# Optimization experiments

Hardware: AMD Instinct MI355X
Metric: run time of the kernel (lower is better)

## Reference

```python
import jax, jax.numpy as jnp
import numpy as np

B, OUT, IN = 4096, 1024, 1024
BN_EPS = 1e-5


def setup_inputs() -> dict:
    key = jax.random.key(0)
    kx, k1, k2, k3 = jax.random.split(key, 4)
    # kaiming_uniform_ with a=sqrt(5): bound = sqrt(6 / ((1+a^2) * fan_in)) = 1/sqrt(fan_in)
    bound = 1.0 / np.sqrt(IN)
    x = jax.random.normal(kx, (B, IN), dtype=jnp.float32)
    c1 = jax.random.uniform(k1, (OUT, IN), jnp.float32, -bound, bound)
    c2 = jax.random.uniform(k2, (OUT, IN), jnp.float32, -bound, bound)
    c3 = jax.random.uniform(k3, (OUT, IN), jnp.float32, -bound, bound)
    bias = jnp.zeros((OUT, IN), jnp.float32)
    gamma = jnp.ones((OUT,), jnp.float32)   # BatchNorm1d weight
    beta = jnp.zeros((OUT,), jnp.float32)   # BatchNorm1d bias
    return {"x": x, "c1": c1, "c2": c2, "c3": c3, "bias": bias,
            "gamma": gamma, "beta": beta}


def reference(x, c1, c2, c3, bias, gamma, beta):
    # Fused polynomial 'matmul': out[b,o] = sum_i x*c1 + x^2*c2 + x^3*c3 + bias
    x2 = x * x
    x3 = x2 * x
    y = (jnp.einsum('bi,oi->bo', x, c1)
         + jnp.einsum('bi,oi->bo', x2, c2)
         + jnp.einsum('bi,oi->bo', x3, c3)
         + jnp.sum(bias, axis=1))  # bias reduced over in_features
    # BatchNorm1d (training mode: batch statistics, biased variance)
    mean = jnp.mean(y, axis=0)
    var = jnp.var(y, axis=0)
    return (y - mean) * jax.lax.rsqrt(var + BN_EPS) * gamma + beta
```

## Files before the change

kernel.cpp:

```cpp
#include <hip/hip_runtime.h>
#include <stdint.h>

#define B_ROWS 4096
#define OUTF   1024
#define INF    1024
#define KTOT   3072
#define BN_EPS 1e-5f
#define BM 128
#define BN 64
#define BK 128

typedef short  short8  __attribute__((ext_vector_type(8)));
typedef float  floatx4 __attribute__((ext_vector_type(4)));

struct alignas(8) s4 { short x, y, z, w; };

__device__ __forceinline__ short f2bf(float f) {
  union { float f; uint32_t u; } cv; cv.f = f;
  uint32_t u = cv.u;
  uint32_t r = (u + 0x7fffu + ((u >> 16) & 1u)) >> 16;
  return (short)r;
}

__device__ __forceinline__ void load_lds16(const void* g, void* l) {
  __builtin_amdgcn_global_load_lds(
      (const __attribute__((address_space(1))) uint32_t*)(uintptr_t)g,
      (__attribute__((address_space(3))) uint32_t*)(uint32_t)(uintptr_t)l,
      16, 0, 0);
}

__global__ void prep_all(const float4* __restrict__ x4,
                         const float4* __restrict__ c1, const float4* __restrict__ c2,
                         const float4* __restrict__ c3, const float* __restrict__ bias,
                         short* __restrict__ Xb, short* __restrict__ Wb,
                         float* __restrict__ biassum) {
  int b = blockIdx.x;
  if (b < 4096) {
    int idx = b * 256 + threadIdx.x;
    float4 v = x4[idx];
    int row = idx >> 8;
    int c   = (idx & 255) << 2;
    size_t base = (size_t)row * KTOT + c;
    s4 p1 = { f2bf(v.x), f2bf(v.y), f2bf(v.z), f2bf(v.w) };
    float ax = v.x * v.x, ay = v.y * v.y, az = v.z * v.z, aw = v.w * v.w;
    s4 p2 = { f2bf(ax), f2bf(ay), f2bf(az), f2bf(aw) };
    s4 p3 = { f2bf(ax * v.x), f2bf(ay * v.y), f2bf(az * v.z), f2bf(aw * v.w) };
    *(s4*)&Xb[base]        = p1;
    *(s4*)&Xb[base + 1024] = p2;
    *(s4*)&Xb[base + 2048] = p3;
  } else if (b < 5120) {
    int idx = (b - 4096) * 256 + threadIdx.x;
    int row = idx >> 8;
    int c   = (idx & 255) << 2;
    size_t base = (size_t)row * KTOT + c;
    float4 a = c1[idx], bb = c2[idx], d = c3[idx];
    s4 p1 = { f2bf(a.x),  f2bf(a.y),  f2bf(a.z),  f2bf(a.w)  };
    s4 p2 = { f2bf(bb.x), f2bf(bb.y), f2bf(bb.z), f2bf(bb.w) };
    s4 p3 = { f2bf(d.x),  f2bf(d.y),  f2bf(d.z),  f2bf(d.w)  };
    *(s4*)&Wb[base]        = p1;
    *(s4*)&Wb[base + 1024] = p2;
    *(s4*)&Wb[base + 2048] = p3;
  } else {
    int o = (b - 5120) * 4 + (threadIdx.x >> 6);
    int l = threadIdx.x & 63;
    const float4* bp = (const float4*)(bias + (size_t)o * INF);
    float s = 0.f;
    for (int i = l; i < 256; i += 64) { float4 v = bp[i]; s += v.x + v.y + v.z + v.w; }
    #pragma unroll
    for (int off = 32; off; off >>= 1) s += __shfl_down(s, off, 64);
    if (l == 0) biassum[o] = s;
  }
}

__global__ __launch_bounds__(256, 2) void gemm_poly(
    const short* __restrict__ Xb, const short* __restrict__ Wb,
    const float* __restrict__ biassum, float* __restrict__ Y,
    float* __restrict__ psum, float* __restrict__ psq) {
  __shared__ __align__(16) short As[BM * BK];
  __shared__ __align__(16) short Bs[BN * BK];
  __shared__ float colred[2][2][BN];
  const int tid  = threadIdx.x;
  const int lane = tid & 63;
  const int wave = tid >> 6;
  const int wr = wave >> 1;
  const int wc = wave & 1;
  const int row0 = blockIdx.y * BM;
  const int col0 = blockIdx.x * BN;
  const short* Ag = Xb + (size_t)row0 * KTOT;
  const short* Bg = Wb + (size_t)col0 * KTOT;
  const int frag_m = lane & 15;
  const int sel = lane >> 4;
  floatx4 acc[4][2] = {};

  int aoff[8], boff[4];
  #pragma unroll
  for (int i = 0; i < 8; ++i) {
    int c = tid + i * 256;
    int r = c >> 4, p = c & 15;
    int l = p ^ (r & 15);
    aoff[i] = r * KTOT + l * 8;
  }
  #pragma unroll
  for (int i = 0; i < 4; ++i) {
    int c = tid + i * 256;
    int r = c >> 4, p = c & 15;
    int l = p ^ (r & 15);
    boff[i] = r * KTOT + l * 8;
  }

  for (int kt = 0; kt < KTOT; kt += BK) {
    #pragma unroll
    for (int i = 0; i < 8; ++i)
      load_lds16(Ag + aoff[i] + kt, &As[(tid + i * 256) * 8]);
    #pragma unroll
    for (int i = 0; i < 4; ++i)
      load_lds16(Bg + boff[i] + kt, &Bs[(tid + i * 256) * 8]);
    __syncthreads();
    #pragma unroll
    for (int s = 0; s < 4; ++s) {
      short8 af[4], bfr[2];
      #pragma unroll
      for (int i = 0; i < 4; ++i) {
        int r = wr * 64 + i * 16 + frag_m;
        int p = (s * 4 + sel) ^ (r & 15);
        af[i] = *(const short8*)&As[r * BK + p * 8];
      }
      #pragma unroll
      for (int j = 0; j < 2; ++j) {
        int r = wc * 32 + j * 16 + frag_m;
        int p = (s * 4 + sel) ^ (r & 15);
        bfr[j] = *(const short8*)&Bs[r * BK + p * 8];
      }
      #pragma unroll
      for (int i = 0; i < 4; ++i)
        #pragma unroll
        for (int j = 0; j < 2; ++j)
          acc[i][j] = __builtin_amdgcn_mfma_f32_16x16x32_bf16(af[i], bfr[j], acc[i][j], 0, 0, 0);
    }
    __syncthreads();
  }

  const int drow = (lane >> 4) << 2;
  const int dcol = lane & 15;
  float s[2] = {0.f, 0.f}, sq[2] = {0.f, 0.f};
  #pragma unroll
  for (int j = 0; j < 2; ++j) {
    int gc = col0 + wc * 32 + j * 16 + dcol;
    float bsv = biassum[gc];
    #pragma unroll
    for (int i = 0; i < 4; ++i) {
      int gr = row0 + wr * 64 + i * 16 + drow;
      #pragma unroll
      for (int r = 0; r < 4; ++r) {
        float v = acc[i][j][r] + bsv;
        Y[(size_t)(gr + r) * OUTF + gc] = v;
        s[j] += v; sq[j] += v * v;
      }
    }
  }
  #pragma unroll
  for (int j = 0; j < 2; ++j) {
    s[j]  += __shfl_xor(s[j], 16, 64);  s[j]  += __shfl_xor(s[j], 32, 64);
    sq[j] += __shfl_xor(sq[j], 16, 64); sq[j] += __shfl_xor(sq[j], 32, 64);
  }
  if (sel == 0) {
    #pragma unroll
    for (int j = 0; j < 2; ++j) {
      int cc = wc * 32 + j * 16 + dcol;
      colred[wr][0][cc] = s[j];
      colred[wr][1][cc] = sq[j];
    }
  }
  __syncthreads();
  if (tid < BN) {
    psum[(size_t)blockIdx.y * OUTF + col0 + tid] = colred[0][0][tid] + colred[1][0][tid];
    psq [(size_t)blockIdx.y * OUTF + col0 + tid] = colred[0][1][tid] + colred[1][1][tid];
  }
}

__global__ void bn_fused(const float* __restrict__ psum, const float* __restrict__ psq,
                         const float* __restrict__ gamma, const float* __restrict__ beta,
                         float* __restrict__ Y) {
  __shared__ float sc[32], sh[32];
  const int c0 = blockIdx.x * 32;
  const int t = threadIdx.x;
  if (t < 32) {
    float s = 0.f, s2 = 0.f;
    #pragma unroll 8
    for (int p = 0; p < 32; ++p) {
      s  += psum[p * OUTF + c0 + t];
      s2 += psq [p * OUTF + c0 + t];
    }
    float mean = s * (1.0f / B_ROWS);
    float var  = s2 * (1.0f / B_ROWS) - mean * mean;
    float scale = gamma[c0 + t] * rsqrtf(var + BN_EPS);
    sc[t] = scale;
    sh[t] = beta[c0 + t] - mean * scale;
  }
  __syncthreads();
  const int f4c = t & 7;
  const int rr  = t >> 3;
  const int row0 = blockIdx.y * 256;
  float4* Y4 = (float4*)Y;
  const int cb = f4c * 4;
  float s0 = sc[cb], s1 = sc[cb+1], s2 = sc[cb+2], s3 = sc[cb+3];
  float h0 = sh[cb], h1 = sh[cb+1], h2 = sh[cb+2], h3 = sh[cb+3];
  #pragma unroll
  for (int it = 0; it < 8; ++it) {
    int row = row0 + it * 32 + rr;
    size_t idx = (size_t)row * 256 + (c0 >> 2) + f4c;
    float4 v = Y4[idx];
    v.x = v.x * s0 + h0; v.y = v.y * s1 + h1;
    v.z = v.z * s2 + h2; v.w = v.w * s3 + h3;
    Y4[idx] = v;
  }
}

extern "C" void kernel_launch(void* const* d_in, const int* in_sizes, int n_in,
                              void* d_out, int out_size, void* d_ws, size_t ws_size,
                              hipStream_t stream) {
  const float* x     = (const float*)d_in[0];
  const float* c1    = (const float*)d_in[1];
  const float* c2    = (const float*)d_in[2];
  const float* c3    = (const float*)d_in[3];
  const float* bias  = (const float*)d_in[4];
  const float* gamma = (const float*)d_in[5];
  const float* beta  = (const float*)d_in[6];
  float* out = (float*)d_out;
  char* ws = (char*)d_ws;

  short* Xb      = (short*)(ws);
  short* Wb      = (short*)(ws + 25165824);
  float* biassum = (float*)(ws + 31457280);
  float* psum    = (float*)(ws + 31461376);
  float* psq     = (float*)(ws + 31592448);

  prep_all<<<5376, 256, 0, stream>>>((const float4*)x, (const float4*)c1,
                                     (const float4*)c2, (const float4*)c3,
                                     bias, Xb, Wb, biassum);

  dim3 ggrid(OUTF / BN, B_ROWS / BM);
  gemm_poly<<<ggrid, 256, 0, stream>>>(Xb, Wb, biassum, out, psum, psq);

  dim3 bgrid(OUTF / 32, B_ROWS / 256);
  bn_fused<<<bgrid, 256, 0, stream>>>(psum, psq, gamma, beta, out);
}
```

Measured before the change: 136.0 us.

## Double-buffer LDS tiles, enlarge GEMM block to 128x128 with XCD-aware tile mapping

The GEMM block tile grows to 128x128 with BK=64 and 512 threads (8 waves), so each block uses more reuse and the grid shrinks to 256 blocks. LDS is double-buffered: the next K-slice is loaded asynchronously while MFMAs run on the current one, and one barrier per step replaces two. Block indices are remapped so consecutive blocks on the same XCD share row tiles, aiming for better L2 locality. The cost is fewer blocks (256 on 256 CUs, about one per CU) and an LDS footprint similar to before.

```diff
diff --git a/kernel.cpp b/kernel.cpp
--- a/kernel.cpp
+++ b/kernel.cpp
@@ -7,8 +7,9 @@
 #define KTOT   3072
 #define BN_EPS 1e-5f
 #define BM 128
-#define BN 64
-#define BK 128
+#define BN 128
+#define BK 64
+#define NSTEP (KTOT / BK)
 
 typedef short  short8  __attribute__((ext_vector_type(8)));
 typedef float  floatx4 __attribute__((ext_vector_type(4)));
@@ -72,64 +73,71 @@
   }
 }
 
-__global__ __launch_bounds__(256, 2) void gemm_poly(
+__global__ __launch_bounds__(512, 2) void gemm_poly(
     const short* __restrict__ Xb, const short* __restrict__ Wb,
     const float* __restrict__ biassum, float* __restrict__ Y,
     float* __restrict__ psum, float* __restrict__ psq) {
-  __shared__ __align__(16) short As[BM * BK];
-  __shared__ __align__(16) short Bs[BN * BK];
-  __shared__ float colred[2][2][BN];
+  __shared__ __align__(16) short As[2][BM * BK];
+  __shared__ __align__(16) short Bs[2][BN * BK];
   const int tid  = threadIdx.x;
   const int lane = tid & 63;
   const int wave = tid >> 6;
-  const int wr = wave >> 1;
-  const int wc = wave & 1;
-  const int row0 = blockIdx.y * BM;
-  const int col0 = blockIdx.x * BN;
+  const int wr = wave >> 2;
+  const int wc = wave & 3;
+  const int lb  = blockIdx.x;
+  const int xcd = lb & 7;
+  const int sl  = lb >> 3;
+  const int bx  = sl & 7;
+  const int by  = xcd * 4 + (sl >> 3);
+  const int row0 = by * BM;
+  const int col0 = bx * BN;
   const short* Ag = Xb + (size_t)row0 * KTOT;
   const short* Bg = Wb + (size_t)col0 * KTOT;
   const int frag_m = lane & 15;
   const int sel = lane >> 4;
   floatx4 acc[4][2] = {};
 
-  int aoff[8], boff[4];
-  #pragma unroll
-  for (int i = 0; i < 8; ++i) {
-    int c = tid + i * 256;
-    int r = c >> 4, p = c & 15;
-    int l = p ^ (r & 15);
-    aoff[i] = r * KTOT + l * 8;
-  }
-  #pragma unroll
-  for (int i = 0; i < 4; ++i) {
-    int c = tid + i * 256;
-    int r = c >> 4, p = c & 15;
-    int l = p ^ (r & 15);
-    boff[i] = r * KTOT + l * 8;
-  }
-
-  for (int kt = 0; kt < KTOT; kt += BK) {
-    #pragma unroll
-    for (int i = 0; i < 8; ++i)
-      load_lds16(Ag + aoff[i] + kt, &As[(tid + i * 256) * 8]);
-    #pragma unroll
-    for (int i = 0; i < 4; ++i)
-      load_lds16(Bg + boff[i] + kt, &Bs[(tid + i * 256) * 8]);
+  int off01[2];
+  #pragma unroll
+  for (int i = 0; i < 2; ++i) {
+    int c = tid + i * 512;
+    int r = c >> 3, p = c & 7;
+    int lg = p ^ (r & 7);
+    off01[i] = r * KTOT + lg * 8;
+  }
+
+  #pragma unroll
+  for (int i = 0; i < 2; ++i) {
+    load_lds16(Ag + off01[i], &As[0][(tid + i * 512) * 8]);
+    load_lds16(Bg + off01[i], &Bs[0][(tid + i * 512) * 8]);
+  }
+
+  for (int step = 0; step < NSTEP; ++step) {
     __syncthreads();
-    #pragma unroll
-    for (int s = 0; s < 4; ++s) {
+    const int cur = step & 1;
+    if (step + 1 < NSTEP) {
+      const int kt = (step + 1) * BK;
+      const int nxt = cur ^ 1;
+      #pragma unroll
+      for (int i = 0; i < 2; ++i) {
+        load_lds16(Ag + off01[i] + kt, &As[nxt][(tid + i * 512) * 8]);
+        load_lds16(Bg + off01[i] + kt, &Bs[nxt][(tid + i * 512) * 8]);
+      }
+    }
+    #pragma unroll
+    for (int s = 0; s < 2; ++s) {
       short8 af[4], bfr[2];
       #pragma unroll
       for (int i = 0; i < 4; ++i) {
         int r = wr * 64 + i * 16 + frag_m;
-        int p = (s * 4 + sel) ^ (r & 15);
-        af[i] = *(const short8*)&As[r * BK + p * 8];
+        int p = (s * 4 + sel) ^ (r & 7);
+        af[i] = *(const short8*)&As[cur][r * BK + p * 8];
       }
       #pragma unroll
       for (int j = 0; j < 2; ++j) {
         int r = wc * 32 + j * 16 + frag_m;
-        int p = (s * 4 + sel) ^ (r & 15);
-        bfr[j] = *(const short8*)&Bs[r * BK + p * 8];
+        int p = (s * 4 + sel) ^ (r & 7);
+        bfr[j] = *(const short8*)&Bs[cur][r * BK + p * 8];
       }
       #pragma unroll
       for (int i = 0; i < 4; ++i)
@@ -137,12 +145,12 @@
         for (int j = 0; j < 2; ++j)
           acc[i][j] = __builtin_amdgcn_mfma_f32_16x16x32_bf16(af[i], bfr[j], acc[i][j], 0, 0, 0);
     }
-    __syncthreads();
-  }
-
-  const int drow = (lane >> 4) << 2;
-  const int dcol = lane & 15;
-  float s[2] = {0.f, 0.f}, sq[2] = {0.f, 0.f};
+  }
+
+  float* colred = (float*)&As[0][0];
+  const int drow = sel << 2;
+  const int dcol = frag_m;
+  float sv[2] = {0.f, 0.f}, sq[2] = {0.f, 0.f};
   #pragma unroll
   for (int j = 0; j < 2; ++j) {
     int gc = col0 + wc * 32 + j * 16 + dcol;
@@ -154,27 +162,29 @@
       for (int r = 0; r < 4; ++r) {
         float v = acc[i][j][r] + bsv;
         Y[(size_t)(gr + r) * OUTF + gc] = v;
-        s[j] += v; sq[j] += v * v;
+        sv[j] += v; sq[j] += v * v;
       }
     }
   }
   #pragma unroll
   for (int j = 0; j < 2; ++j) {
-    s[j]  += __shfl_xor(s[j], 16, 64);  s[j]  += __shfl_xor(s[j], 32, 64);
+    sv[j] += __shfl_xor(sv[j], 16, 64); sv[j] += __shfl_xor(sv[j], 32, 64);
     sq[j] += __shfl_xor(sq[j], 16, 64); sq[j] += __shfl_xor(sq[j], 32, 64);
   }
   if (sel == 0) {
     #pragma unroll
     for (int j = 0; j < 2; ++j) {
       int cc = wc * 32 + j * 16 + dcol;
-      colred[wr][0][cc] = s[j];
-      colred[wr][1][cc] = sq[j];
+      colred[wr * 256 + cc]       = sv[j];
+      colred[wr * 256 + 128 + cc] = sq[j];
     }
   }
   __syncthreads();
   if (tid < BN) {
-    psum[(size_t)blockIdx.y * OUTF + col0 + tid] = colred[0][0][tid] + colred[1][0][tid];
-    psq [(size_t)blockIdx.y * OUTF + col0 + tid] = colred[0][1][tid] + colred[1][1][tid];
+    float ssum = colred[tid]       + colred[256 + tid];
+    float ssq  = colred[128 + tid] + colred[384 + tid];
+    psum[(size_t)by * OUTF + col0 + tid] = ssum;
+    psq [(size_t)by * OUTF + col0 + tid] = ssq;
   }
 }
 
@@ -239,8 +249,7 @@
                                      (const float4*)c2, (const float4*)c3,
                                      bias, Xb, Wb, biassum);
 
-  dim3 ggrid(OUTF / BN, B_ROWS / BM);
-  gemm_poly<<<ggrid, 256, 0, stream>>>(Xb, Wb, biassum, out, psum, psq);
+  gemm_poly<<<256, 512, 0, stream>>>(Xb, Wb, biassum, out, psum, psq);
 
   dim3 bgrid(OUTF / 32, B_ROWS / 256);
   bn_fused<<<bgrid, 256, 0, stream>>>(psum, psq, gamma, beta, out);
```

Measured after the change: 130.7 us. 1.04x faster.
